# Optimization experiments

Measured on AMD Instinct MI355X. Metric: run time of the kernel, lower is better.

The kernel has to match this reference:

```python
import jax, jax.numpy as jnp
import numpy as np

B, T, D, H, HID = 1024, 128, 256, 512, 512
INITIAL_DT = 0.01
DT = 0.1  # uniform spacing of x_time -> n_tp == 1 every step (single Euler step)


def setup_inputs() -> dict:
    key = jax.random.key(0)
    ks = jax.random.split(key, 13)
    g = lambda k, shp, sc: (jax.random.normal(k, shp, dtype=jnp.float32) * sc)
    C = 2 * H + D  # GRU input: concat(h_mean, h_std, x)
    return {
        "x": jax.random.normal(ks[0], (B, T, D), dtype=jnp.float32),
        "x_time": jnp.arange(T, dtype=jnp.float32) * DT,
        # ODE func f(h): 2-layer tanh MLP
        "W1": g(ks[1], (H, HID), 1.0 / np.sqrt(H)),
        "b1": jnp.zeros((HID,), jnp.float32),
        "W2": g(ks[2], (HID, H), 1.0 / np.sqrt(HID)),
        "b2": jnp.zeros((H,), jnp.float32),
        # GRU unit (latent-ODE style): update gate, reset gate, new-state net
        "Wz": g(ks[3], (C, H), 1.0 / np.sqrt(C)),
        "bz": jnp.zeros((H,), jnp.float32),
        "Wr": g(ks[4], (C, H), 1.0 / np.sqrt(C)),
        "br": jnp.zeros((H,), jnp.float32),
        "Wn": g(ks[5], (C, 2 * H), 1.0 / np.sqrt(C)),
        "bn": jnp.zeros((2 * H,), jnp.float32),
    }


def reference(x, x_time, W1, b1, W2, b2, Wz, bz, Wr, br, Wn, bn):
    Bsz = x.shape[0]
    Hd = W1.shape[0]
    h0 = jnp.zeros((Bsz, Hd), x.dtype)
    std0 = jnp.zeros((Bsz, Hd), x.dtype)
    t0 = x_time[0] - INITIAL_DT

    def ode_f(h):  # dh/dt (autonomous MLP, as diffeq_solver ODE func)
        return jnp.tanh(h @ W1 + b1) @ W2 + b2

    def step(carry, inp):
        h, hstd, t_prev = carry
        xi, ti = inp
        dt = ti - t_prev
        # one Euler step of the ODE solver (n_tp<=1 for uniform x_time)
        h_ode = h + ode_f(h) * dt
        # GRU unit on (h_ode, hstd, xi)
        cat = jnp.concatenate([h_ode, hstd, xi], axis=-1)  # [B, 2H+D]
        z = jax.nn.sigmoid(cat @ Wz + bz)
        r = jax.nn.sigmoid(cat @ Wr + br)
        cat_r = jnp.concatenate([h_ode * r, hstd * r, xi], axis=-1)
        n_mean, n_std = jnp.split(cat_r @ Wn + bn, 2, axis=-1)
        n_std = jnp.abs(n_std)
        h_new = (1.0 - z) * n_mean + z * h_ode
        std_new = jnp.abs((1.0 - z) * n_std + z * hstd)
        return (h_new, std_new, ti), None

    xs = (jnp.swapaxes(x, 0, 1), x_time)  # [T,B,D], [T]
    (hT, stdT, _), _ = jax.lax.scan(step, (h0, std0, t0), xs)
    return hT, stdT
```

## Files before the change

kernel.cpp:

```cpp
#include <hip/hip_runtime.h>
#include <hip/hip_bf16.h>

#define B_SZ 1024
#define T_SZ 128
#define D_SZ 256
#define H_SZ 512
#define NBLK 256
#define NTHR 512
#define AUXS 0x0

typedef __attribute__((ext_vector_type(8))) short short8;
typedef __attribute__((ext_vector_type(4))) float f32x4;

__device__ inline f32x4 mfma16(short8 a, short8 b, f32x4 c) {
  return __builtin_amdgcn_mfma_f32_16x16x32_bf16(a, b, c, 0, 0, 0);
}

__device__ inline void st_bf16(__hip_bfloat16* p, float v) {
  union { __hip_bfloat16 b; unsigned short u; } cv;
  cv.b = __float2bfloat16(v);
  unsigned int vv = cv.u;
  asm volatile("global_store_short %0, %1, off" :: "v"(p), "v"(vv) : "memory");
}

#define INV()                                        \
  do {                                               \
    asm volatile("buffer_inv sc0" ::: "memory");     \
    __builtin_amdgcn_sched_barrier(0);               \
  } while (0)

template <int ROWS, int AUX>
__device__ __forceinline__ void stage512(const __hip_bfloat16* __restrict__ src,
                                         int strideElts, int row0, int k0,
                                         unsigned short* lds, int tid) {
  constexpr int CH = ROWS * 8;
#pragma unroll
  for (int it = 0; it * NTHR < CH; ++it) {
    int wbase = it * NTHR + ((tid >> 6) << 6);
    if (wbase < CH) {
      int chunk = it * NTHR + tid;
      int row = chunk >> 3, slot = chunk & 7;
      int ksrc = (slot ^ (row & 7)) << 3;
      const __hip_bfloat16* g = src + (size_t)(row0 + row) * strideElts + (k0 + ksrc);
      unsigned short* l = lds + (size_t)wbase * 8;
      __builtin_amdgcn_global_load_lds(
          (const __attribute__((address_space(1))) unsigned int*)g,
          (__attribute__((address_space(3))) unsigned int*)l, 16, 0, AUX);
    }
  }
}

__device__ __forceinline__ short8 ldfrag(const unsigned short* lds, int row, int slot) {
  int s = slot ^ (row & 7);
  return *(const short8*)(lds + row * 64 + s * 8);
}

template <int NT, int PB, typename SA, typename SB, typename CC>
__device__ __forceinline__ void gloop(int wv, SA sa, SB sb, CC cc) {
  sa(0, 0); sa(1, 1); sa(2, 2); sa(3, 3);
#pragma unroll 1
  for (int kt = 0; kt < NT; ++kt) {
    if (wv < 4) {
      if (kt == 0)           asm volatile("s_waitcnt vmcnt(3)" ::: "memory");
      else if (kt == 1)      asm volatile("s_waitcnt vmcnt(%0)" :: "i"(3 + PB) : "memory");
      else if (kt <= NT - 4) asm volatile("s_waitcnt vmcnt(%0)" :: "i"(3 + 2 * PB) : "memory");
      else if (kt == NT - 3) asm volatile("s_waitcnt vmcnt(%0)" :: "i"(2 + 2 * PB) : "memory");
      else if (kt == NT - 2) asm volatile("s_waitcnt vmcnt(%0)" :: "i"(1 + PB) : "memory");
      else                   asm volatile("s_waitcnt vmcnt(0)" ::: "memory");
    } else {
      if (kt <= NT - 3)      asm volatile("s_waitcnt vmcnt(%0)" :: "i"(2 * PB) : "memory");
      else if (kt == NT - 2) asm volatile("s_waitcnt vmcnt(%0)" :: "i"(PB) : "memory");
      else                   asm volatile("s_waitcnt vmcnt(0)" ::: "memory");
    }
    __builtin_amdgcn_s_barrier();
    __builtin_amdgcn_sched_barrier(0);
    if (kt + 3 < NT) sb(kt + 3, (kt + 3) & 3);
    if (kt + 4 < NT) sa(kt + 4, (kt + 4) % 5);
    cc(kt % 5, kt & 3);
  }
}

__device__ __forceinline__ void sbar_arrive(unsigned* scnt) {
  asm volatile("s_waitcnt vmcnt(0)" ::: "memory");
  __syncthreads();
  if (threadIdx.x == 0)
    __hip_atomic_fetch_add(scnt, 1u, __ATOMIC_RELAXED, __HIP_MEMORY_SCOPE_AGENT);
}
__device__ __forceinline__ void sbar_wait(unsigned* scnt, unsigned p) {
  if (threadIdx.x == 0) {
    while (__hip_atomic_load(scnt, __ATOMIC_RELAXED, __HIP_MEMORY_SCOPE_AGENT) < p * 8u)
      __builtin_amdgcn_s_sleep(1);
  }
  __syncthreads();
  __builtin_amdgcn_sched_barrier(0);
}

__global__ __launch_bounds__(512, 2) void k_fused(
    const float* __restrict__ xg, const float* __restrict__ xtime,
    const __hip_bfloat16* __restrict__ W1t, const float* __restrict__ b1,
    const __hip_bfloat16* __restrict__ W2t, const float* __restrict__ b2,
    const __hip_bfloat16* __restrict__ Wzrt, const float* __restrict__ bz,
    const float* __restrict__ br, const __hip_bfloat16* __restrict__ Wnt,
    const float* __restrict__ bn, float* __restrict__ hf, float* __restrict__ hstdf,
    __hip_bfloat16* __restrict__ hbf, __hip_bfloat16* __restrict__ Ubf,
    __hip_bfloat16* __restrict__ hodeb, __hip_bfloat16* __restrict__ hstdb,
    __hip_bfloat16* __restrict__ A4, __hip_bfloat16* __restrict__ xstep,
    unsigned* __restrict__ bar) {
  __shared__ __align__(16) unsigned short lA[5][32 * 64];
  __shared__ __align__(16) unsigned short lB[4][128 * 64];
  int tid = threadIdx.x, lane = tid & 63, wv = tid >> 6;
  int lr = lane & 15, lg = lane >> 4;
  int rh = wv >> 2, cq = wv & 3;
  int b = blockIdx.x;
  int xcd = b & 7;
  int j = b >> 3;
  int i = (xcd << 2) | (j >> 3);
  int s = j & 7;
  int m0 = i << 5;
  int nA = s << 6;
  unsigned* scnt = bar + i * 32;
  unsigned p = 0;
  int cl = (cq << 4) + lr;
  int col = nA + cl;
  int row0 = m0 + (rh << 4) + (lg << 2);
  float hreg[4] = {0.f, 0.f, 0.f, 0.f}, sreg[4] = {0.f, 0.f, 0.f, 0.f};
  float oreg[4], zreg[4];

  stage512<64, 0>(W1t, H_SZ, nA, 0, lB[0], tid);
  stage512<64, 0>(W1t, H_SZ, nA, 64, lB[1], tid);
  stage512<64, 0>(W1t, H_SZ, nA, 128, lB[2], tid);

#pragma unroll 1
  for (int t = 0; t < T_SZ; ++t) {
    {
      f32x4 acc = {};
      auto sa = [&](int kt, int bi) { stage512<32, AUXS>(hbf, H_SZ, m0, kt << 6, lA[bi], tid); };
      auto sb = [&](int kt, int bi) { stage512<64, 0>(W1t, H_SZ, nA, kt << 6, lB[bi], tid); };
      auto cc = [&](int ai, int bi) {
#pragma unroll
        for (int kk = 0; kk < 2; ++kk) {
          short8 a = ldfrag(lA[ai], (rh << 4) + lr, (kk << 2) + lg);
          short8 bb = ldfrag(lB[bi], cl, (kk << 2) + lg);
          acc = mfma16(a, bb, acc);
        }
      };
      gloop<8, 1>(wv, sa, sb, cc);
      float bi = b1[col];
#pragma unroll
      for (int r = 0; r < 4; ++r)
        st_bf16(&Ubf[(size_t)(row0 + r) * H_SZ + col], tanhf(acc[r] + bi));
    }
    sbar_arrive(scnt);
    stage512<64, 0>(W2t, H_SZ, nA, 0, lB[0], tid);
    stage512<64, 0>(W2t, H_SZ, nA, 64, lB[1], tid);
    stage512<64, 0>(W2t, H_SZ, nA, 128, lB[2], tid);
    sbar_wait(scnt, ++p);
    INV();
    {
      f32x4 acc = {};
      auto sa = [&](int kt, int bi) { stage512<32, AUXS>(Ubf, H_SZ, m0, kt << 6, lA[bi], tid); };
      auto sb = [&](int kt, int bi) { stage512<64, 0>(W2t, H_SZ, nA, kt << 6, lB[bi], tid); };
      auto cc = [&](int ai, int bi) {
#pragma unroll
        for (int kk = 0; kk < 2; ++kk) {
          short8 a = ldfrag(lA[ai], (rh << 4) + lr, (kk << 2) + lg);
          short8 bb = ldfrag(lB[bi], cl, (kk << 2) + lg);
          acc = mfma16(a, bb, acc);
        }
      };
      gloop<8, 1>(wv, sa, sb, cc);
      float dtv = (t == 0) ? 0.01f : (xtime[t] - xtime[t - 1]);
      float bi = b2[col];
#pragma unroll
      for (int r = 0; r < 4; ++r) {
        float v = hreg[r] + dtv * (acc[r] + bi);
        oreg[r] = v;
        st_bf16(&hodeb[(size_t)(row0 + r) * H_SZ + col], v);
      }
      {
        int colx = (s << 5) + (tid & 31);
#pragma unroll
        for (int it2 = 0; it2 < 2; ++it2) {
          int row = m0 + (tid >> 5) + (it2 << 4);
          float xv = xg[((size_t)row * T_SZ + t) * D_SZ + colx];
          st_bf16(&xstep[(size_t)row * D_SZ + colx], xv);
        }
      }
    }
    sbar_arrive(scnt);
#pragma unroll
    for (int q = 0; q < 3; ++q) {
      stage512<64, 0>(Wzrt, 1280, nA, q << 6, lB[q], tid);
      stage512<64, 0>(Wzrt, 1280, 512 + nA, q << 6, lB[q] + 64 * 64, tid);
    }
    sbar_wait(scnt, ++p);
    INV();
    {
      f32x4 acc0 = {}, acc1 = {};
      auto sa = [&](int kt, int bi) {
        int ke = kt << 6;
        if (ke < 512)       stage512<32, AUXS>(hodeb, H_SZ, m0, ke, lA[bi], tid);
        else if (ke < 1024) stage512<32, AUXS>(hstdb, H_SZ, m0, ke - 512, lA[bi], tid);
        else                stage512<32, AUXS>(xstep, D_SZ, m0, ke - 1024, lA[bi], tid);
      };
      auto sb = [&](int kt, int bi) {
        stage512<64, 0>(Wzrt, 1280, nA, kt << 6, lB[bi], tid);
        stage512<64, 0>(Wzrt, 1280, 512 + nA, kt << 6, lB[bi] + 64 * 64, tid);
      };
      auto cc = [&](int ai, int bi) {
#pragma unroll
        for (int kk = 0; kk < 2; ++kk) {
          short8 a = ldfrag(lA[ai], (rh << 4) + lr, (kk << 2) + lg);
          short8 b0 = ldfrag(lB[bi], cl, (kk << 2) + lg);
          short8 b1f = ldfrag(lB[bi], 64 + cl, (kk << 2) + lg);
          acc0 = mfma16(a, b0, acc0);
          acc1 = mfma16(a, b1f, acc1);
        }
      };
      gloop<20, 2>(wv, sa, sb, cc);
      float bz_ = bz[col], br_ = br[col];
#pragma unroll
      for (int r = 0; r < 4; ++r) {
        int row = row0 + r;
        zreg[r] = 1.f / (1.f + expf(-(acc0[r] + bz_)));
        float g = 1.f / (1.f + expf(-(acc1[r] + br_)));
        st_bf16(&A4[(size_t)row * 1024 + col], oreg[r] * g);
        st_bf16(&A4[(size_t)row * 1024 + 512 + col], sreg[r] * g);
      }
    }
    sbar_arrive(scnt);
#pragma unroll
    for (int q = 0; q < 3; ++q) {
      stage512<64, 0>(Wnt, 1280, nA, q << 6, lB[q], tid);
      stage512<64, 0>(Wnt, 1280, 512 + nA, q << 6, lB[q] + 64 * 64, tid);
    }
    sbar_wait(scnt, ++p);
    INV();
    {
      f32x4 acc0 = {}, acc1 = {};
      auto sa = [&](int kt, int bi) {
        int ke = kt << 6;
        if (ke < 1024) stage512<32, AUXS>(A4, 1024, m0, ke, lA[bi], tid);
        else           stage512<32, AUXS>(xstep, D_SZ, m0, ke - 1024, lA[bi], tid);
      };
      auto sb = [&](int kt, int bi) {
        stage512<64, 0>(Wnt, 1280, nA, kt << 6, lB[bi], tid);
        stage512<64, 0>(Wnt, 1280, 512 + nA, kt << 6, lB[bi] + 64 * 64, tid);
      };
      auto cc = [&](int ai, int bi) {
#pragma unroll
        for (int kk = 0; kk < 2; ++kk) {
          short8 a = ldfrag(lA[ai], (rh << 4) + lr, (kk << 2) + lg);
          short8 b0 = ldfrag(lB[bi], cl, (kk << 2) + lg);
          short8 b1f = ldfrag(lB[bi], 64 + cl, (kk << 2) + lg);
          acc0 = mfma16(a, b0, acc0);
          acc1 = mfma16(a, b1f, acc1);
        }
      };
      gloop<20, 2>(wv, sa, sb, cc);
      float bm = bn[col], bs = bn[512 + col];
#pragma unroll
      for (int r = 0; r < 4; ++r) {
        int row = row0 + r;
        float z = zreg[r];
        float hn = (1.f - z) * (acc0[r] + bm) + z * oreg[r];
        hreg[r] = hn;
        st_bf16(&hbf[(size_t)row * H_SZ + col], hn);
        float ns = fabsf(acc1[r] + bs);
        float sn = fabsf((1.f - z) * ns + z * sreg[r]);
        sreg[r] = sn;
        st_bf16(&hstdb[(size_t)row * H_SZ + col], sn);
      }
    }
    sbar_arrive(scnt);
    stage512<64, 0>(W1t, H_SZ, nA, 0, lB[0], tid);
    stage512<64, 0>(W1t, H_SZ, nA, 64, lB[1], tid);
    stage512<64, 0>(W1t, H_SZ, nA, 128, lB[2], tid);
    sbar_wait(scnt, ++p);
    INV();
  }
#pragma unroll
  for (int r = 0; r < 4; ++r) {
    int row = row0 + r;
    hf[(size_t)row * H_SZ + col] = hreg[r];
    hstdf[(size_t)row * H_SZ + col] = sreg[r];
  }
}

__global__ void k_wt(const float* __restrict__ W, __hip_bfloat16* __restrict__ Wt,
                     int K, int N, int ld) {
  size_t i = (size_t)blockIdx.x * 256 + threadIdx.x;
  if (i >= (size_t)K * N) return;
  int n = (int)(i / K), k = (int)(i % K);
  Wt[(size_t)n * ld + k] = __float2bfloat16(W[(size_t)k * N + n]);
}

extern "C" void kernel_launch(void* const* d_in, const int* in_sizes, int n_in,
                              void* d_out, int out_size, void* d_ws, size_t ws_size,
                              hipStream_t stream) {
  const float* x     = (const float*)d_in[0];
  const float* xtime = (const float*)d_in[1];
  const float* W1    = (const float*)d_in[2];
  const float* b1    = (const float*)d_in[3];
  const float* W2    = (const float*)d_in[4];
  const float* b2    = (const float*)d_in[5];
  const float* Wz    = (const float*)d_in[6];
  const float* bz    = (const float*)d_in[7];
  const float* Wr    = (const float*)d_in[8];
  const float* br    = (const float*)d_in[9];
  const float* Wn    = (const float*)d_in[10];
  const float* bn    = (const float*)d_in[11];

  char* p = (char*)d_ws;
  __hip_bfloat16* W1t   = (__hip_bfloat16*)(p + 0);
  __hip_bfloat16* W2t   = (__hip_bfloat16*)(p + 524288);
  __hip_bfloat16* Wzrt  = (__hip_bfloat16*)(p + 1048576);
  __hip_bfloat16* Wnt   = (__hip_bfloat16*)(p + 3670016);
  float*          hf    = (float*)(p + 6291456);
  float*          hstdf = (float*)(p + 8388608);
  __hip_bfloat16* hbf   = (__hip_bfloat16*)(p + 14680064);
  __hip_bfloat16* Ubf   = (__hip_bfloat16*)(p + 15728640);
  __hip_bfloat16* hodeb = (__hip_bfloat16*)(p + 16777216);
  __hip_bfloat16* hstdb = (__hip_bfloat16*)(p + 17825792);
  __hip_bfloat16* A4    = (__hip_bfloat16*)(p + 18874368);
  __hip_bfloat16* xstep = (__hip_bfloat16*)(p + 20971520);
  unsigned*       bar   = (unsigned*)(p + 21495808);

  hipMemsetAsync(hbf, 0, 1048576, stream);
  hipMemsetAsync(hstdb, 0, 1048576, stream);
  hipMemsetAsync(bar, 0, 8192, stream);

  k_wt<<<(512 * 512 + 255) / 256, 256, 0, stream>>>(W1, W1t, 512, 512, 512);
  k_wt<<<(512 * 512 + 255) / 256, 256, 0, stream>>>(W2, W2t, 512, 512, 512);
  k_wt<<<(1280 * 512 + 255) / 256, 256, 0, stream>>>(Wz, Wzrt, 1280, 512, 1280);
  k_wt<<<(1280 * 512 + 255) / 256, 256, 0, stream>>>(Wr, Wzrt + (size_t)512 * 1280, 1280, 512, 1280);
  k_wt<<<(1280 * 1024 + 255) / 256, 256, 0, stream>>>(Wn, Wnt, 1280, 1024, 1280);

  k_fused<<<NBLK, NTHR, 0, stream>>>(x, xtime, W1t, b1, W2t, b2, Wzrt, bz, br,
                                     Wnt, bn, hf, hstdf, hbf, Ubf,
                                     hodeb, hstdb, A4, xstep, bar);

  hipMemcpyAsync(d_out, hf, 2097152, hipMemcpyDeviceToDevice, stream);
  hipMemcpyAsync((char*)d_out + 2097152, hstdf, 2097152, hipMemcpyDeviceToDevice, stream);
}
```

Before: 4.980 ms.

## Double K-tile depth to 128 with 3-stage weight ring and single-block occupancy

Widens each K tile from 64 to 128 elements, so every pipeline iteration stages twice as much data and issues twice as many MFMAs. The loop runs half as many iterations and hits half as many barriers. The weight ring drops from four buffers to three with a prefetch distance of two, and the vmcnt wait schedule is rebuilt to be uniform across all waves. LDS use grows to about 160KB, so launch bounds fall to one block per CU. This trades occupancy and latency hiding for fewer synchronisations per GEMM phase.

```diff
diff --git a/kernel.cpp b/kernel.cpp
--- a/kernel.cpp
+++ b/kernel.cpp
@@ -7,7 +7,6 @@
 #define H_SZ 512
 #define NBLK 256
 #define NTHR 512
-#define AUXS 0x0
 
 typedef __attribute__((ext_vector_type(8))) short short8;
 typedef __attribute__((ext_vector_type(4))) float f32x4;
@@ -30,17 +29,17 @@
   } while (0)
 
 template <int ROWS, int AUX>
-__device__ __forceinline__ void stage512(const __hip_bfloat16* __restrict__ src,
-                                         int strideElts, int row0, int k0,
-                                         unsigned short* lds, int tid) {
-  constexpr int CH = ROWS * 8;
+__device__ __forceinline__ void stageW(const __hip_bfloat16* __restrict__ src,
+                                       int strideElts, int row0, int k0,
+                                       unsigned short* lds, int tid) {
+  constexpr int CH = ROWS * 16;
 #pragma unroll
   for (int it = 0; it * NTHR < CH; ++it) {
     int wbase = it * NTHR + ((tid >> 6) << 6);
     if (wbase < CH) {
       int chunk = it * NTHR + tid;
-      int row = chunk >> 3, slot = chunk & 7;
-      int ksrc = (slot ^ (row & 7)) << 3;
+      int row = chunk >> 4, sl = chunk & 15;
+      int ksrc = (sl ^ (row & 7)) << 3;
       const __hip_bfloat16* g = src + (size_t)(row0 + row) * strideElts + (k0 + ksrc);
       unsigned short* l = lds + (size_t)wbase * 8;
       __builtin_amdgcn_global_load_lds(
@@ -50,33 +49,27 @@
   }
 }
 
-__device__ __forceinline__ short8 ldfrag(const unsigned short* lds, int row, int slot) {
+__device__ __forceinline__ short8 ldf(const unsigned short* buf, int row, int slot) {
   int s = slot ^ (row & 7);
-  return *(const short8*)(lds + row * 64 + s * 8);
+  return *(const short8*)(buf + row * 128 + (s << 3));
 }
 
 template <int NT, int PB, typename SA, typename SB, typename CC>
-__device__ __forceinline__ void gloop(int wv, SA sa, SB sb, CC cc) {
+__device__ __forceinline__ void gloop(SA sa, SB sb, CC cc) {
   sa(0, 0); sa(1, 1); sa(2, 2); sa(3, 3);
 #pragma unroll 1
   for (int kt = 0; kt < NT; ++kt) {
-    if (wv < 4) {
-      if (kt == 0)           asm volatile("s_waitcnt vmcnt(3)" ::: "memory");
-      else if (kt == 1)      asm volatile("s_waitcnt vmcnt(%0)" :: "i"(3 + PB) : "memory");
-      else if (kt <= NT - 4) asm volatile("s_waitcnt vmcnt(%0)" :: "i"(3 + 2 * PB) : "memory");
-      else if (kt == NT - 3) asm volatile("s_waitcnt vmcnt(%0)" :: "i"(2 + 2 * PB) : "memory");
-      else if (kt == NT - 2) asm volatile("s_waitcnt vmcnt(%0)" :: "i"(1 + PB) : "memory");
-      else                   asm volatile("s_waitcnt vmcnt(0)" ::: "memory");
-    } else {
-      if (kt <= NT - 3)      asm volatile("s_waitcnt vmcnt(%0)" :: "i"(2 * PB) : "memory");
-      else if (kt == NT - 2) asm volatile("s_waitcnt vmcnt(%0)" :: "i"(PB) : "memory");
-      else                   asm volatile("s_waitcnt vmcnt(0)" ::: "memory");
-    }
+    if (kt == 0)           asm volatile("s_waitcnt vmcnt(3)" ::: "memory");
+    else if (kt == 1)      asm volatile("s_waitcnt vmcnt(%0)" :: "i"(2 + PB + (NT > 4 ? 1 : 0)) : "memory");
+    else if (kt <= NT - 4) asm volatile("s_waitcnt vmcnt(%0)" :: "i"(2 + PB) : "memory");
+    else if (kt == NT - 3) asm volatile("s_waitcnt vmcnt(%0)" :: "i"(1 + PB) : "memory");
+    else if (kt == NT - 2) asm volatile("s_waitcnt vmcnt(%0)" :: "i"(PB) : "memory");
+    else                   asm volatile("s_waitcnt vmcnt(0)" ::: "memory");
     __builtin_amdgcn_s_barrier();
     __builtin_amdgcn_sched_barrier(0);
-    if (kt + 3 < NT) sb(kt + 3, (kt + 3) & 3);
+    if (kt + 2 < NT) sb(kt + 2, (kt + 2) % 3);
     if (kt + 4 < NT) sa(kt + 4, (kt + 4) % 5);
-    cc(kt % 5, kt & 3);
+    cc(kt % 5, kt % 3);
   }
 }
 
@@ -95,7 +88,7 @@
   __builtin_amdgcn_sched_barrier(0);
 }
 
-__global__ __launch_bounds__(512, 2) void k_fused(
+__global__ __launch_bounds__(512, 1) void k_fused(
     const float* __restrict__ xg, const float* __restrict__ xtime,
     const __hip_bfloat16* __restrict__ W1t, const float* __restrict__ b1,
     const __hip_bfloat16* __restrict__ W2t, const float* __restrict__ b2,
@@ -106,8 +99,8 @@
     __hip_bfloat16* __restrict__ hodeb, __hip_bfloat16* __restrict__ hstdb,
     __hip_bfloat16* __restrict__ A4, __hip_bfloat16* __restrict__ xstep,
     unsigned* __restrict__ bar) {
-  __shared__ __align__(16) unsigned short lA[5][32 * 64];
-  __shared__ __align__(16) unsigned short lB[4][128 * 64];
+  __shared__ __align__(16) unsigned short lA[5][32 * 128];
+  __shared__ __align__(16) unsigned short lB[3][128 * 128];
   int tid = threadIdx.x, lane = tid & 63, wv = tid >> 6;
   int lr = lane & 15, lg = lane >> 4;
   int rh = wv >> 2, cq = wv & 3;
@@ -126,49 +119,48 @@
   float hreg[4] = {0.f, 0.f, 0.f, 0.f}, sreg[4] = {0.f, 0.f, 0.f, 0.f};
   float oreg[4], zreg[4];
 
-  stage512<64, 0>(W1t, H_SZ, nA, 0, lB[0], tid);
-  stage512<64, 0>(W1t, H_SZ, nA, 64, lB[1], tid);
-  stage512<64, 0>(W1t, H_SZ, nA, 128, lB[2], tid);
+  INV();
+  stageW<64, 0>(W1t, H_SZ, nA, 0, lB[0], tid);
+  stageW<64, 0>(W1t, H_SZ, nA, 128, lB[1], tid);
 
 #pragma unroll 1
   for (int t = 0; t < T_SZ; ++t) {
     {
       f32x4 acc = {};
-      auto sa = [&](int kt, int bi) { stage512<32, AUXS>(hbf, H_SZ, m0, kt << 6, lA[bi], tid); };
-      auto sb = [&](int kt, int bi) { stage512<64, 0>(W1t, H_SZ, nA, kt << 6, lB[bi], tid); };
+      auto sa = [&](int kt, int bi) { stageW<32, 0>(hbf, H_SZ, m0, kt << 7, lA[bi], tid); };
+      auto sb = [&](int kt, int bi) { stageW<64, 0>(W1t, H_SZ, nA, kt << 7, lB[bi], tid); };
       auto cc = [&](int ai, int bi) {
 #pragma unroll
-        for (int kk = 0; kk < 2; ++kk) {
-          short8 a = ldfrag(lA[ai], (rh << 4) + lr, (kk << 2) + lg);
-          short8 bb = ldfrag(lB[bi], cl, (kk << 2) + lg);
+        for (int kk = 0; kk < 4; ++kk) {
+          short8 a = ldf(lA[ai], (rh << 4) + lr, (kk << 2) + lg);
+          short8 bb = ldf(lB[bi], cl, (kk << 2) + lg);
           acc = mfma16(a, bb, acc);
         }
       };
-      gloop<8, 1>(wv, sa, sb, cc);
+      gloop<4, 2>(sa, sb, cc);
       float bi = b1[col];
 #pragma unroll
       for (int r = 0; r < 4; ++r)
         st_bf16(&Ubf[(size_t)(row0 + r) * H_SZ + col], tanhf(acc[r] + bi));
     }
     sbar_arrive(scnt);
-    stage512<64, 0>(W2t, H_SZ, nA, 0, lB[0], tid);
-    stage512<64, 0>(W2t, H_SZ, nA, 64, lB[1], tid);
-    stage512<64, 0>(W2t, H_SZ, nA, 128, lB[2], tid);
+    stageW<64, 0>(W2t, H_SZ, nA, 0, lB[0], tid);
+    stageW<64, 0>(W2t, H_SZ, nA, 128, lB[1], tid);
     sbar_wait(scnt, ++p);
     INV();
     {
       f32x4 acc = {};
-      auto sa = [&](int kt, int bi) { stage512<32, AUXS>(Ubf, H_SZ, m0, kt << 6, lA[bi], tid); };
-      auto sb = [&](int kt, int bi) { stage512<64, 0>(W2t, H_SZ, nA, kt << 6, lB[bi], tid); };
+      auto sa = [&](int kt, int bi) { stageW<32, 0>(Ubf, H_SZ, m0, kt << 7, lA[bi], tid); };
+      auto sb = [&](int kt, int bi) { stageW<64, 0>(W2t, H_SZ, nA, kt << 7, lB[bi], tid); };
       auto cc = [&](int ai, int bi) {
 #pragma unroll
-        for (int kk = 0; kk < 2; ++kk) {
-          short8 a = ldfrag(lA[ai], (rh << 4) + lr, (kk << 2) + lg);
-          short8 bb = ldfrag(lB[bi], cl, (kk << 2) + lg);
+        for (int kk = 0; kk < 4; ++kk) {
+          short8 a = ldf(lA[ai], (rh << 4) + lr, (kk << 2) + lg);
+          short8 bb = ldf(lB[bi], cl, (kk << 2) + lg);
           acc = mfma16(a, bb, acc);
         }
       };
-      gloop<8, 1>(wv, sa, sb, cc);
+      gloop<4, 2>(sa, sb, cc);
       float dtv = (t == 0) ? 0.01f : (xtime[t] - xtime[t - 1]);
       float bi = b2[col];
 #pragma unroll
@@ -189,35 +181,35 @@
     }
     sbar_arrive(scnt);
 #pragma unroll
-    for (int q = 0; q < 3; ++q) {
-      stage512<64, 0>(Wzrt, 1280, nA, q << 6, lB[q], tid);
-      stage512<64, 0>(Wzrt, 1280, 512 + nA, q << 6, lB[q] + 64 * 64, tid);
+    for (int q = 0; q < 2; ++q) {
+      stageW<64, 0>(Wzrt, 1280, nA, q << 7, lB[q], tid);
+      stageW<64, 0>(Wzrt, 1280, 512 + nA, q << 7, lB[q] + 64 * 128, tid);
     }
     sbar_wait(scnt, ++p);
     INV();
     {
       f32x4 acc0 = {}, acc1 = {};
       auto sa = [&](int kt, int bi) {
-        int ke = kt << 6;
-        if (ke < 512)       stage512<32, AUXS>(hodeb, H_SZ, m0, ke, lA[bi], tid);
-        else if (ke < 1024) stage512<32, AUXS>(hstdb, H_SZ, m0, ke - 512, lA[bi], tid);
-        else                stage512<32, AUXS>(xstep, D_SZ, m0, ke - 1024, lA[bi], tid);
+        int ke = kt << 7;
+        if (ke < 512)       stageW<32, 0>(hodeb, H_SZ, m0, ke, lA[bi], tid);
+        else if (ke < 1024) stageW<32, 0>(hstdb, H_SZ, m0, ke - 512, lA[bi], tid);
+        else                stageW<32, 0>(xstep, D_SZ, m0, ke - 1024, lA[bi], tid);
       };
       auto sb = [&](int kt, int bi) {
-        stage512<64, 0>(Wzrt, 1280, nA, kt << 6, lB[bi], tid);
-        stage512<64, 0>(Wzrt, 1280, 512 + nA, kt << 6, lB[bi] + 64 * 64, tid);
+        stageW<64, 0>(Wzrt, 1280, nA, kt << 7, lB[bi], tid);
+        stageW<64, 0>(Wzrt, 1280, 512 + nA, kt << 7, lB[bi] + 64 * 128, tid);
       };
       auto cc = [&](int ai, int bi) {
 #pragma unroll
-        for (int kk = 0; kk < 2; ++kk) {
-          short8 a = ldfrag(lA[ai], (rh << 4) + lr, (kk << 2) + lg);
-          short8 b0 = ldfrag(lB[bi], cl, (kk << 2) + lg);
-          short8 b1f = ldfrag(lB[bi], 64 + cl, (kk << 2) + lg);
+        for (int kk = 0; kk < 4; ++kk) {
+          short8 a = ldf(lA[ai], (rh << 4) + lr, (kk << 2) + lg);
+          short8 b0 = ldf(lB[bi], cl, (kk << 2) + lg);
+          short8 b1f = ldf(lB[bi] + 64 * 128, cl, (kk << 2) + lg);
           acc0 = mfma16(a, b0, acc0);
           acc1 = mfma16(a, b1f, acc1);
         }
       };
-      gloop<20, 2>(wv, sa, sb, cc);
+      gloop<10, 4>(sa, sb, cc);
       float bz_ = bz[col], br_ = br[col];
 #pragma unroll
       for (int r = 0; r < 4; ++r) {
@@ -230,34 +222,34 @@
     }
     sbar_arrive(scnt);
 #pragma unroll
-    for (int q = 0; q < 3; ++q) {
-      stage512<64, 0>(Wnt, 1280, nA, q << 6, lB[q], tid);
-      stage512<64, 0>(Wnt, 1280, 512 + nA, q << 6, lB[q] + 64 * 64, tid);
+    for (int q = 0; q < 2; ++q) {
+      stageW<64, 0>(Wnt, 1280, nA, q << 7, lB[q], tid);
+      stageW<64, 0>(Wnt, 1280, 512 + nA, q << 7, lB[q] + 64 * 128, tid);
     }
     sbar_wait(scnt, ++p);
     INV();
     {
       f32x4 acc0 = {}, acc1 = {};
       auto sa = [&](int kt, int bi) {
-        int ke = kt << 6;
-        if (ke < 1024) stage512<32, AUXS>(A4, 1024, m0, ke, lA[bi], tid);
-        else           stage512<32, AUXS>(xstep, D_SZ, m0, ke - 1024, lA[bi], tid);
+        int ke = kt << 7;
+        if (ke < 1024) stageW<32, 0>(A4, 1024, m0, ke, lA[bi], tid);
+        else           stageW<32, 0>(xstep, D_SZ, m0, ke - 1024, lA[bi], tid);
       };
       auto sb = [&](int kt, int bi) {
-        stage512<64, 0>(Wnt, 1280, nA, kt << 6, lB[bi], tid);
-        stage512<64, 0>(Wnt, 1280, 512 + nA, kt << 6, lB[bi] + 64 * 64, tid);
+        stageW<64, 0>(Wnt, 1280, nA, kt << 7, lB[bi], tid);
+        stageW<64, 0>(Wnt, 1280, 512 + nA, kt << 7, lB[bi] + 64 * 128, tid);
       };
       auto cc = [&](int ai, int bi) {
 #pragma unroll
-        for (int kk = 0; kk < 2; ++kk) {
-          short8 a = ldfrag(lA[ai], (rh << 4) + lr, (kk << 2) + lg);
-          short8 b0 = ldfrag(lB[bi], cl, (kk << 2) + lg);
-          short8 b1f = ldfrag(lB[bi], 64 + cl, (kk << 2) + lg);
+        for (int kk = 0; kk < 4; ++kk) {
+          short8 a = ldf(lA[ai], (rh << 4) + lr, (kk << 2) + lg);
+          short8 b0 = ldf(lB[bi], cl, (kk << 2) + lg);
+          short8 b1f = ldf(lB[bi] + 64 * 128, cl, (kk << 2) + lg);
           acc0 = mfma16(a, b0, acc0);
           acc1 = mfma16(a, b1f, acc1);
         }
       };
-      gloop<20, 2>(wv, sa, sb, cc);
+      gloop<10, 4>(sa, sb, cc);
       float bm = bn[col], bs = bn[512 + col];
 #pragma unroll
       for (int r = 0; r < 4; ++r) {
@@ -273,9 +265,8 @@
       }
     }
     sbar_arrive(scnt);
-    stage512<64, 0>(W1t, H_SZ, nA, 0, lB[0], tid);
-    stage512<64, 0>(W1t, H_SZ, nA, 64, lB[1], tid);
-    stage512<64, 0>(W1t, H_SZ, nA, 128, lB[2], tid);
+    stageW<64, 0>(W1t, H_SZ, nA, 0, lB[0], tid);
+    stageW<64, 0>(W1t, H_SZ, nA, 128, lB[1], tid);
     sbar_wait(scnt, ++p);
     INV();
   }
```

Measured after the change: 4.165 ms. 1.2x faster.
